# Optimization experiments

Measured on AMD Instinct MI355X. Metric: run time of the kernel, lower is better.

The kernel has to match this reference:

```python
import jax, jax.numpy as jnp
import numpy as np

N_PTS = 65536   # input points
M = 4096        # sampled clusters (n_nodes)
K = 16          # knn neighbors
C_IN = 128
C_OUT = 256
BN_EPS = 1e-5


def setup_inputs() -> dict:
    key = jax.random.key(0)
    k1, k2, k3 = jax.random.split(key, 3)
    x = jax.random.normal(k1, (N_PTS, C_IN), jnp.float32)
    pos = jax.random.normal(k2, (N_PTS, 3), jnp.float32)
    batch = jnp.zeros((N_PTS,), jnp.int32)  # single point cloud
    W = jax.random.normal(k3, (C_IN, C_OUT), jnp.float32) / np.sqrt(C_IN)
    b = jnp.zeros((C_OUT,), jnp.float32)
    gamma = jnp.ones((C_OUT,), jnp.float32)
    beta = jnp.zeros((C_OUT,), jnp.float32)
    return {"x": x, "pos": pos, "batch": batch, "W": W, "b": b,
            "gamma": gamma, "beta": beta}


def _fps(pos, m):
    """Farthest point sampling starting from index 0. Returns m indices."""
    n = pos.shape[0]

    def step(carry, _):
        min_d, last = carry
        d = jnp.sum((pos - pos[last]) ** 2, axis=-1)  # [N]
        min_d = jnp.minimum(min_d, d)
        nxt = jnp.argmax(min_d).astype(jnp.int32)
        return (min_d, nxt), nxt

    init = (jnp.full((n,), jnp.inf, pos.dtype), jnp.int32(0))
    _, rest = jax.lax.scan(step, init, None, length=m - 1)
    return jnp.concatenate([jnp.zeros((1,), jnp.int32), rest])


def _knn(pos, sub_pos, k):
    """For each of M query points, indices of k nearest points in pos. [M, k]"""
    # squared euclidean distances, [M, N]
    d2 = (jnp.sum(sub_pos ** 2, -1, keepdims=True)
          - 2.0 * sub_pos @ pos.T
          + jnp.sum(pos ** 2, -1)[None, :])
    _, idx = jax.lax.top_k(-d2, k)
    return idx


def _mlp(x, W, b, gamma, beta):
    # Linear -> BatchNorm1d (training-mode batch stats, biased var) -> ReLU
    h = x @ W + b                      # [N, C_OUT]
    mu = jnp.mean(h, axis=0)
    var = jnp.mean((h - mu) ** 2, axis=0)
    h = gamma * (h - mu) * jax.lax.rsqrt(var + BN_EPS) + beta
    return jax.nn.relu(h)


def reference(x, pos, batch, W, b, gamma, beta):
    id_clusters = _fps(pos, M)                 # [M]
    sub_pos = pos[id_clusters]                 # [M, 3]
    sub_batch = batch[id_clusters]             # [M]
    nbr = _knn(pos, sub_pos, K)                # [M, K]
    h = _mlp(x, W, b, gamma, beta)             # [N, C_OUT]
    # gather + max-pool over each cluster's k neighbors (== scatter_max,
    # since knn emits exactly K neighbors per cluster, grouped by cluster)
    out = jnp.max(h[nbr], axis=1)              # [M, C_OUT]
    return out, sub_pos, sub_batch
```

## Files before the change

### kernel.cpp

```cpp
#include <hip/hip_runtime.h>
#include <hip/hip_bf16.h>

#define N_PTS 65536
#define MCLUS 4096
#define KNN   16
#define C_IN  128
#define C_OUT 256

typedef unsigned long long u64;
typedef unsigned u32;

#define WS_ID     0
#define WS_SLOTS  16384
#define WS_NBR    49152
#define WS_PSUM   311296
#define WS_PSUMSQ 835584
#define WS_SCALE  1359872
#define WS_SHIFT  1360896

__global__ void init_kernel(int* __restrict__ id, u64* __restrict__ slots) {
    int t = threadIdx.x;
    for (int i = t; i < 4096; i += 1024) slots[i] = 0ull;
    if (t == 0) id[0] = 0;
}

__device__ __forceinline__ float dist3(float ax, float ay, float az,
                                       float bx, float by, float bz) {
    float dx = __fsub_rn(ax, bx), dy = __fsub_rn(ay, by), dz = __fsub_rn(az, bz);
    return __fadd_rn(__fadd_rn(__fmul_rn(dx, dx), __fmul_rn(dy, dy)), __fmul_rn(dz, dz));
}

__device__ __forceinline__ u32 wave_max_u32(u32 v) {
    #pragma unroll
    for (int off = 32; off > 0; off >>= 1) {
        u32 o = __shfl_xor(v, off);
        v = o > v ? o : v;
    }
    return v;
}

__device__ __forceinline__ int wave_argmax48(u64 k48) {
    u32 hi = (u32)(k48 >> 16);
    u32 him = wave_max_u32(hi);
    u64 ball = __ballot(hi == him);
    if (__popcll(ball) > 1) {
        u32 a = (hi == him) ? (u32)(k48 & 0xFFFFull) : 0u;
        u32 am = wave_max_u32(a);
        ball = __ballot((hi == him) && (a == am));
    }
    return __ffsll((long long)ball) - 1;
}

__global__ __launch_bounds__(64) void fps_kernel(const float* __restrict__ pos,
                                                 int* __restrict__ id,
                                                 u64* __restrict__ slots) {
    const int lane = threadIdx.x;
    const int blk  = blockIdx.x;
    __shared__ float bku[1024];

    float px[16], py[16], pz[16], md[16];
    const float c0x = pos[0], c0y = pos[1], c0z = pos[2];
    #pragma unroll
    for (int e = 0; e < 16; ++e) {
        int gi = blk * 1024 + e * 64 + lane;
        px[e] = pos[gi * 3 + 0]; py[e] = pos[gi * 3 + 1]; pz[e] = pos[gi * 3 + 2];
        md[e] = dist3(px[e], py[e], pz[e], c0x, c0y, c0z);
    }

    int r = 0;
    bool pending = false;

    auto slow_round = [&](int rr, int s) {
        u64 bk = 0; float bx = 0.f, by = 0.f, bz = 0.f;
        #pragma unroll
        for (int e = 0; e < 16; ++e) {
            u32 inv = 0xFFFFu - (u32)(blk * 1024 + e * 64 + lane);
            u64 k = ((u64)__float_as_uint(md[e]) << 16) | inv;
            bool bt = k > bk;
            bk = bt ? k : bk; bx = bt ? px[e] : bx; by = bt ? py[e] : by; bz = bt ? pz[e] : bz;
        }
        int src = wave_argmax48(bk);
        float wx = __shfl(bx, src), wy = __shfl(by, src), wz = __shfl(bz, src);
        u64 kb = __shfl(bk, src);

        const u64 tg = (u64)((rr + 1) & 0xFFFF);
        u64* base = &slots[(u32)(rr & 1) * 2048];
        {
            u64 w0 = (kb << 16) | tg;
            u64 w1 = ((u64)__float_as_uint(wx) << 32) | tg;
            u64 w2 = ((u64)__float_as_uint(wy) << 32) | tg;
            u64 w3 = ((u64)__float_as_uint(wz) << 32) | tg;
            u64 wv = (lane == 0) ? w0 : (lane == 1) ? w1 : (lane == 2) ? w2 : w3;
            if (lane < 4)
                __hip_atomic_store(&base[(u32)blk * 32 + (u32)lane], wv,
                                   __ATOMIC_RELAXED, __HIP_MEMORY_SCOPE_AGENT);
        }
        u64* bp = &base[(u32)lane * 32];
        u64 v0, v1, v2, v3;
        for (;;) {
            v0 = __hip_atomic_load(&bp[0], __ATOMIC_RELAXED, __HIP_MEMORY_SCOPE_AGENT);
            v1 = __hip_atomic_load(&bp[1], __ATOMIC_RELAXED, __HIP_MEMORY_SCOPE_AGENT);
            v2 = __hip_atomic_load(&bp[2], __ATOMIC_RELAXED, __HIP_MEMORY_SCOPE_AGENT);
            v3 = __hip_atomic_load(&bp[3], __ATOMIC_RELAXED, __HIP_MEMORY_SCOPE_AGENT);
            u64 bad = ((v0 ^ tg) | (v1 ^ tg) | (v2 ^ tg) | (v3 ^ tg)) & 0xFFFFull;
            if (bad == 0ull) break;
        }
        u64 k2 = v0 >> 16;
        int s2 = wave_argmax48(k2);
        u64 kw = __shfl(k2, s2);
        float cx = __shfl(__uint_as_float((u32)(v1 >> 32)), s2);
        float cy = __shfl(__uint_as_float((u32)(v2 >> 32)), s2);
        float cz = __shfl(__uint_as_float((u32)(v3 >> 32)), s2);
        if (blk == 0 && lane == 0) id[s] = (int)(0xFFFFu - (u32)(kw & 0xFFFFull));
        #pragma unroll
        for (int e = 0; e < 16; ++e)
            md[e] = fminf(md[e], dist3(px[e], py[e], pz[e], cx, cy, cz));
    };

    for (int B = 0; B <= 511; ++B) {
        u64 bk = 0; float bx = 0.f, by = 0.f, bz = 0.f;
        #pragma unroll
        for (int e = 0; e < 16; ++e) {
            u32 inv = 0xFFFFu - (u32)(blk * 1024 + e * 64 + lane);
            u64 k = ((u64)__float_as_uint(md[e]) << 16) | inv;
            bool bt = k > bk;
            bk = bt ? k : bk; bx = bt ? px[e] : bx; by = bt ? py[e] : by; bz = bt ? pz[e] : bz;
        }
        u64 ks = bk;
        #pragma unroll
        for (int off = 1; off <= 4; off <<= 1) {
            u64 o = __shfl_xor(ks, off);
            if (o > ks) ks = o;
        }
        {
            u64 ball = __ballot(bk == ks);
            int segbase = (lane >> 3) << 3;
            int ssrc = __ffsll((long long)(ball & (0xFFull << segbase))) - 1;
            bx = __shfl(bx, ssrc); by = __shfl(by, ssrc); bz = __shfl(bz, ssrc);
        }

        const u64 tg = (u64)((r + 1) & 0xFFFF);
        u64* base = &slots[(u32)(r & 1) * 2048];
        {
            int c = lane / 3; if (c > 7) c = 7;
            int p = lane - c * 3;
            int srcl = 8 * c;
            u64 kk  = __shfl(ks, srcl);
            float gx = __shfl(bx, srcl), gy = __shfl(by, srcl), gz = __shfl(bz, srcl);
            u32 hi, mid;
            if (p == 0)      { hi = __float_as_uint(gx); mid = (u32)(kk & 0xFFFFull); }
            else if (p == 1) { hi = __float_as_uint(gy); mid = (u32)(kk >> 32) & 0xFFFFu; }
            else             { hi = __float_as_uint(gz); mid = (u32)(kk >> 16) & 0xFFFFu; }
            u64 wd = ((u64)hi << 32) | ((u64)mid << 16) | tg;
            if (lane == 24) wd = ((u64)(pending ? 1u : 0u) << 16) | tg;
            if (lane < 25)
                __hip_atomic_store(&base[(u32)blk * 32 + (u32)lane], wd,
                                   __ATOMIC_RELAXED, __HIP_MEMORY_SCOPE_AGENT);
        }

        u64 w[25]; u32 valid = 0;
        {
            u64* bp = &base[(u32)lane * 32];
            do {
                #pragma unroll
                for (int i = 0; i < 25; ++i)
                    if (!(valid & (1u << i)))
                        w[i] = __hip_atomic_load(&bp[i], __ATOMIC_RELAXED, __HIP_MEMORY_SCOPE_AGENT);
                #pragma unroll
                for (int i = 0; i < 25; ++i)
                    if ((u32)(w[i] & 0xFFFFull) == (u32)tg) valid |= (1u << i);
            } while (valid != 0x1FFFFFFu);
        }
        ++r;

        bool anyviol = (__ballot(((w[24] >> 16) & 1ull) != 0ull) != 0ull);
        if (anyviol) {
            #pragma unroll
            for (int e = 0; e < 16; ++e) md[e] = bku[e * 64 + lane];
            int sbase = 8 * (B - 1) + 1;
            for (int sub = 0; sub < 8; ++sub) { slow_round(r, sbase + sub); ++r; }
            pending = false;
            --B; continue;
        }
        if (B == 511) break;

        float cpx[8], cpy[8], cpz[8], cmdf[8]; u32 cinv[8];
        #pragma unroll
        for (int c = 0; c < 8; ++c) {
            u64 a = w[3 * c], b = w[3 * c + 1], d = w[3 * c + 2];
            cpx[c] = __uint_as_float((u32)(a >> 32));
            cpy[c] = __uint_as_float((u32)(b >> 32));
            cpz[c] = __uint_as_float((u32)(d >> 32));
            cinv[c] = (u32)(a >> 16) & 0xFFFFu;
            u32 mdb = (((u32)(b >> 16) & 0xFFFFu) << 16) | ((u32)(d >> 16) & 0xFFFFu);
            cmdf[c] = __uint_as_float(mdb);
        }

        u64 wk48[8]; float wxa[8], wya[8], wza[8];
        float pwx = 0.f, pwy = 0.f, pwz = 0.f;
        #pragma unroll
        for (int j = 0; j < 8; ++j) {
            if (j) {
                #pragma unroll
                for (int c = 0; c < 8; ++c)
                    cmdf[c] = fminf(cmdf[c], dist3(cpx[c], cpy[c], cpz[c], pwx, pwy, pwz));
            }
            u64 bk2 = 0; float b2x = 0.f, b2y = 0.f, b2z = 0.f;
            #pragma unroll
            for (int c = 0; c < 8; ++c) {
                u64 k = ((u64)__float_as_uint(cmdf[c]) << 16) | cinv[c];
                bool bt = k > bk2;
                bk2 = bt ? k : bk2; b2x = bt ? cpx[c] : b2x; b2y = bt ? cpy[c] : b2y; b2z = bt ? cpz[c] : b2z;
            }
            int src = wave_argmax48(bk2);
            u64 kw = __shfl(bk2, src);
            float wx = __shfl(b2x, src), wy = __shfl(b2y, src), wz = __shfl(b2z, src);
            wk48[j] = kw; wxa[j] = wx; wya[j] = wy; wza[j] = wz;
            pwx = wx; pwy = wy; pwz = wz;
            if (blk == 0 && lane == 0) id[8 * B + 1 + j] = (int)(0xFFFFu - (u32)(kw & 0xFFFFull));
        }

        #pragma unroll
        for (int e = 0; e < 16; ++e) bku[e * 64 + lane] = md[e];
        bool viol = false;
        #pragma unroll
        for (int j = 0; j < 8; ++j) {
            #pragma unroll
            for (int e = 0; e < 16; ++e) {
                u32 inv = 0xFFFFu - (u32)(blk * 1024 + e * 64 + lane);
                u64 vk = ((u64)__float_as_uint(md[e]) << 16) | inv;
                viol |= (vk > wk48[j]);
            }
            #pragma unroll
            for (int e = 0; e < 16; ++e)
                md[e] = fminf(md[e], dist3(px[e], py[e], pz[e], wxa[j], wya[j], wza[j]));
        }
        pending = (__ballot(viol) != 0ull);
    }

    for (int s = 4089; s < 4096; ++s) { slow_round(r, s); ++r; }
}

__global__ void subout_kernel(const float* __restrict__ pos, const int* __restrict__ batch,
                              const int* __restrict__ id, float* __restrict__ sub_pos,
                              int* __restrict__ sub_batch) {
    int m = blockIdx.x * blockDim.x + threadIdx.x;
    if (m >= MCLUS) return;
    int idx = id[m];
    sub_pos[m*3+0] = pos[idx*3+0];
    sub_pos[m*3+1] = pos[idx*3+1];
    sub_pos[m*3+2] = pos[idx*3+2];
    sub_batch[m] = batch[idx];
}

__global__ __launch_bounds__(64) void knn_kernel(const float* __restrict__ pos,
                                                 const int* __restrict__ id,
                                                 int* __restrict__ nbr) {
    const int q = blockIdx.x;
    const int lane = threadIdx.x;
    const int qi = id[q];
    const float qx = pos[qi*3+0], qy = pos[qi*3+1], qz = pos[qi*3+2];
    const float nq = __fadd_rn(__fadd_rn(__fmul_rn(qx,qx), __fmul_rn(qy,qy)), __fmul_rn(qz,qz));

    float dl[KNN]; int il[KNN];
    #pragma unroll
    for (int t = 0; t < KNN; ++t) { dl[t] = __builtin_inff(); il[t] = 0x7FFFFFFF; }

    for (int j = lane; j < N_PTS; j += 64) {
        float px = pos[j*3+0], py = pos[j*3+1], pz = pos[j*3+2];
        float npj = __fadd_rn(__fadd_rn(__fmul_rn(px,px), __fmul_rn(py,py)), __fmul_rn(pz,pz));
        float dot = __fadd_rn(__fadd_rn(__fmul_rn(qx,px), __fmul_rn(qy,py)), __fmul_rn(qz,pz));
        float d2  = __fadd_rn(__fsub_rn(nq, __fmul_rn(2.0f, dot)), npj);
        if (d2 < dl[KNN-1] || (d2 == dl[KNN-1] && j < il[KNN-1])) {
            dl[KNN-1] = d2; il[KNN-1] = j;
            #pragma unroll
            for (int t = KNN-1; t > 0; --t) {
                float a = dl[t-1], bq = dl[t];
                int   ai = il[t-1], bi = il[t];
                bool sw = (bq < a) || (bq == a && bi < ai);
                dl[t-1] = sw ? bq : a;  dl[t] = sw ? a : bq;
                il[t-1] = sw ? bi : ai; il[t] = sw ? ai : bi;
            }
        }
    }

    __shared__ float sd[64][KNN];
    __shared__ int   si[64][KNN];
    #pragma unroll
    for (int t = 0; t < KNN; ++t) { sd[lane][t] = dl[t]; si[lane][t] = il[t]; }
    __syncthreads();

    int ptr = 0;
    for (int rr = 0; rr < KNN; ++rr) {
        unsigned long long key = ~0ull;
        if (ptr < KNN) {
            unsigned u = __float_as_uint(sd[lane][ptr]);
            unsigned mu = (u >> 31) ? ~u : (u | 0x80000000u);
            key = ((unsigned long long)mu << 32) | (unsigned)si[lane][ptr];
        }
        unsigned long long m = key;
        #pragma unroll
        for (int off = 32; off > 0; off >>= 1) {
            unsigned long long o = __shfl_xor(m, off);
            if (o < m) m = o;
        }
        if (key == m) ptr++;
        if (lane == 0) nbr[q*KNN + rr] = (int)(m & 0xFFFFFFFFull);
    }
}

__global__ __launch_bounds__(256) void stats_kernel(const float* __restrict__ x,
                                                    const float* __restrict__ W,
                                                    const float* __restrict__ b,
                                                    float* __restrict__ psum,
                                                    float* __restrict__ psumsq) {
    __shared__ float xl[64*128];
    const int tid = threadIdx.x;
    const int cg = (tid & 63) * 4;
    const int rq = tid >> 6;
    float s0=0,s1=0,s2v=0,s3=0, q0=0,q1=0,q2=0,q3=0;
    const float4 bv = *(const float4*)&b[cg];

    for (int t = 0; t < 2; ++t) {
        const size_t row0 = (size_t)blockIdx.x*128 + (size_t)t*64;
        __syncthreads();
        for (int i = tid*4; i < 64*128; i += 1024)
            *(float4*)&xl[i] = *(const float4*)&x[row0*128 + i];
        __syncthreads();

        float acc[16][4];
        #pragma unroll
        for (int rr = 0; rr < 16; ++rr) { acc[rr][0]=bv.x; acc[rr][1]=bv.y; acc[rr][2]=bv.z; acc[rr][3]=bv.w; }

        for (int k4 = 0; k4 < 32; ++k4) {
            float4 w0 = *(const float4*)&W[(k4*4+0)*256 + cg];
            float4 w1 = *(const float4*)&W[(k4*4+1)*256 + cg];
            float4 w2 = *(const float4*)&W[(k4*4+2)*256 + cg];
            float4 w3 = *(const float4*)&W[(k4*4+3)*256 + cg];
            #pragma unroll
            for (int rr = 0; rr < 16; ++rr) {
                float4 xv = *(float4*)&xl[(rq*16+rr)*128 + k4*4];
                acc[rr][0] = fmaf(xv.w,w3.x, fmaf(xv.z,w2.x, fmaf(xv.y,w1.x, fmaf(xv.x,w0.x, acc[rr][0]))));
                acc[rr][1] = fmaf(xv.w,w3.y, fmaf(xv.z,w2.y, fmaf(xv.y,w1.y, fmaf(xv.x,w0.y, acc[rr][1]))));
                acc[rr][2] = fmaf(xv.w,w3.z, fmaf(xv.z,w2.z, fmaf(xv.y,w1.z, fmaf(xv.x,w0.z, acc[rr][2]))));
                acc[rr][3] = fmaf(xv.w,w3.w, fmaf(xv.z,w2.w, fmaf(xv.y,w1.w, fmaf(xv.x,w0.w, acc[rr][3]))));
            }
        }
        #pragma unroll
        for (int rr = 0; rr < 16; ++rr) {
            s0 += acc[rr][0]; q0 = fmaf(acc[rr][0],acc[rr][0],q0);
            s1 += acc[rr][1]; q1 = fmaf(acc[rr][1],acc[rr][1],q1);
            s2v+= acc[rr][2]; q2 = fmaf(acc[rr][2],acc[rr][2],q2);
            s3 += acc[rr][3]; q3 = fmaf(acc[rr][3],acc[rr][3],q3);
        }
    }
    __syncthreads();
    float* red = xl;
    red[rq*256 + cg+0] = s0; red[rq*256 + cg+1] = s1; red[rq*256 + cg+2] = s2v; red[rq*256 + cg+3] = s3;
    red[1024 + rq*256 + cg+0] = q0; red[1024 + rq*256 + cg+1] = q1;
    red[1024 + rq*256 + cg+2] = q2; red[1024 + rq*256 + cg+3] = q3;
    __syncthreads();
    if (rq == 0) {
        #pragma unroll
        for (int c = 0; c < 4; ++c) {
            int ch = cg + c;
            float ss = red[ch] + red[256+ch] + red[512+ch] + red[768+ch];
            float qq = red[1024+ch] + red[1280+ch] + red[1536+ch] + red[1792+ch];
            psum  [blockIdx.x*256 + ch] = ss;
            psumsq[blockIdx.x*256 + ch] = qq;
        }
    }
}

__global__ void finalize_kernel(const float* __restrict__ psum, const float* __restrict__ psumsq,
                                const float* __restrict__ gamma, const float* __restrict__ beta,
                                float* __restrict__ scale, float* __restrict__ shift) {
    int c = threadIdx.x;
    float s = 0.f, s2 = 0.f;
    for (int bl = 0; bl < 512; ++bl) { s += psum[bl*256+c]; s2 += psumsq[bl*256+c]; }
    float mu  = s  / 65536.0f;
    float var = s2 / 65536.0f - mu*mu;
    float inv = rsqrtf(var + 1e-5f);
    float sc = gamma[c] * inv;
    scale[c] = sc;
    shift[c] = beta[c] - mu * sc;
}

__global__ __launch_bounds__(256) void out_kernel(const float* __restrict__ x,
                                                  const float* __restrict__ W,
                                                  const float* __restrict__ b,
                                                  const int* __restrict__ nbr,
                                                  const float* __restrict__ scale,
                                                  const float* __restrict__ shift,
                                                  float* __restrict__ out) {
    __shared__ float xl[16*128];
    __shared__ int nb[16];
    const int tid = threadIdx.x;
    const int m = blockIdx.x;
    if (tid < 16) nb[tid] = nbr[m*16 + tid];
    __syncthreads();
    for (int i = tid; i < 16*128; i += 256) {
        int rr = i >> 7, k = i & 127;
        xl[i] = x[(size_t)nb[rr]*128 + k];
    }
    __syncthreads();

    float acc[16];
    const float bias = b[tid];
    #pragma unroll
    for (int rr = 0; rr < 16; ++rr) acc[rr] = bias;

    for (int k4 = 0; k4 < 32; ++k4) {
        float w0 = W[(k4*4+0)*256 + tid];
        float w1 = W[(k4*4+1)*256 + tid];
        float w2 = W[(k4*4+2)*256 + tid];
        float w3 = W[(k4*4+3)*256 + tid];
        #pragma unroll
        for (int rr = 0; rr < 16; ++rr) {
            float4 xv = *(float4*)&xl[rr*128 + k4*4];
            acc[rr] = fmaf(xv.w,w3, fmaf(xv.z,w2, fmaf(xv.y,w1, fmaf(xv.x,w0, acc[rr]))));
        }
    }
    const float sc = scale[tid], sh = shift[tid];
    float v = acc[0];
    #pragma unroll
    for (int rr = 1; rr < 16; ++rr) v = (sc >= 0.f) ? fmaxf(v, acc[rr]) : fminf(v, acc[rr]);
    out[(size_t)m*256 + tid] = fmaxf(fmaf(sc, v, sh), 0.f);
}

extern "C" void kernel_launch(void* const* d_in, const int* in_sizes, int n_in,
                              void* d_out, int out_size, void* d_ws, size_t ws_size,
                              hipStream_t stream) {
    const float* x     = (const float*)d_in[0];
    const float* pos   = (const float*)d_in[1];
    const int*   batch = (const int*)  d_in[2];
    const float* W     = (const float*)d_in[3];
    const float* b     = (const float*)d_in[4];
    const float* gamma = (const float*)d_in[5];
    const float* beta  = (const float*)d_in[6];

    float* out      = (float*)d_out;
    float* sub_pos  = out + (size_t)MCLUS*C_OUT;
    int*   sub_batch= (int*)(out + (size_t)MCLUS*C_OUT + (size_t)MCLUS*3);

    char* ws = (char*)d_ws;
    int* id        = (int*)(ws + WS_ID);
    u64* slots     = (u64*)(ws + WS_SLOTS);
    int* nbr       = (int*)(ws + WS_NBR);
    float* psum    = (float*)(ws + WS_PSUM);
    float* psumsq  = (float*)(ws + WS_PSUMSQ);
    float* scalep  = (float*)(ws + WS_SCALE);
    float* shiftp  = (float*)(ws + WS_SHIFT);

    init_kernel<<<1, 1024, 0, stream>>>(id, slots);
    fps_kernel<<<64, 64, 0, stream>>>(pos, id, slots);
    subout_kernel<<<16, 256, 0, stream>>>(pos, batch, id, sub_pos, sub_batch);
    knn_kernel<<<MCLUS, 64, 0, stream>>>(pos, id, nbr);
    stats_kernel<<<512, 256, 0, stream>>>(x, W, b, psum, psumsq);
    finalize_kernel<<<1, 256, 0, stream>>>(psum, psumsq, gamma, beta, scalep, shiftp);
    out_kernel<<<MCLUS, 256, 0, stream>>>(x, W, b, nbr, scalep, shiftp, out);
}
```

Before: 7.569 ms.

## Spatially sort each FPS block's points into k-d cells before sampling

At kernel start, each FPS block sorts its 1024 points with three nested bitonic sorts in shared memory, by x, then y, then z, building a k-d style partition. Each 8-lane segment then holds a spatially compact group of points, and the original indices are precomputed for tie-breaking. The likely aim is to make the speculative per-segment candidate selection in the batched FPS loop more accurate, so fewer rounds hit violations and fall back to the slow path. The cost is an upfront sort with many __syncthreads barriers, extra shared memory, and 16 more registers per lane for the index array.

```diff
diff --git a/kernel.cpp b/kernel.cpp
--- a/kernel.cpp
+++ b/kernel.cpp
@@ -51,19 +51,70 @@
     return __ffsll((long long)ball) - 1;
 }
 
+__device__ __forceinline__ u32 fkey(float v) {
+    u32 u = __float_as_uint(v);
+    return (u >> 31) ? ~u : (u | 0x80000000u);
+}
+
+__device__ __forceinline__ void bsort_seg(u64* arr, int segsize, int lane) {
+    const int half = segsize >> 1;
+    for (int k = 2; k <= segsize; k <<= 1) {
+        for (int j = k >> 1; j > 0; j >>= 1) {
+            for (int t = lane; t < 512; t += 64) {
+                int seg = t / half;
+                int tt  = t - seg * half;
+                int io  = ((tt & ~(j - 1)) << 1) | (tt & (j - 1));
+                int i   = seg * segsize + io;
+                int l   = i | j;
+                u64 a = arr[i], b = arr[l];
+                bool up = ((io & k) == 0);
+                if ((a > b) == up) { arr[i] = b; arr[l] = a; }
+            }
+            __syncthreads();
+        }
+    }
+}
+
 __global__ __launch_bounds__(64) void fps_kernel(const float* __restrict__ pos,
                                                  int* __restrict__ id,
                                                  u64* __restrict__ slots) {
     const int lane = threadIdx.x;
     const int blk  = blockIdx.x;
+    __shared__ float sx[1024], sy[1024], sz[1024];
+    __shared__ u64  arr[1024];
     __shared__ float bku[1024];
 
+    for (int p = lane; p < 1024; p += 64) {
+        int gi = blk * 1024 + p;
+        sx[p] = pos[gi * 3 + 0]; sy[p] = pos[gi * 3 + 1]; sz[p] = pos[gi * 3 + 2];
+    }
+    __syncthreads();
+    for (int p = lane; p < 1024; p += 64)
+        arr[p] = ((u64)fkey(sx[p]) << 32) | (u32)p;
+    __syncthreads();
+    bsort_seg(arr, 1024, lane);
+    for (int p = lane; p < 1024; p += 64) {
+        u32 li = (u32)(arr[p] & 0xFFFFull);
+        arr[p] = ((u64)fkey(sy[li]) << 32) | li;
+    }
+    __syncthreads();
+    bsort_seg(arr, 512, lane);
+    for (int p = lane; p < 1024; p += 64) {
+        u32 li = (u32)(arr[p] & 0xFFFFull);
+        arr[p] = ((u64)fkey(sz[li]) << 32) | li;
+    }
+    __syncthreads();
+    bsort_seg(arr, 256, lane);
+
     float px[16], py[16], pz[16], md[16];
+    u32 inv[16];
     const float c0x = pos[0], c0y = pos[1], c0z = pos[2];
     #pragma unroll
     for (int e = 0; e < 16; ++e) {
-        int gi = blk * 1024 + e * 64 + lane;
-        px[e] = pos[gi * 3 + 0]; py[e] = pos[gi * 3 + 1]; pz[e] = pos[gi * 3 + 2];
+        int sp = (lane >> 3) * 128 + e * 8 + (lane & 7);
+        u32 li = (u32)(arr[sp] & 0xFFFFull);
+        px[e] = sx[li]; py[e] = sy[li]; pz[e] = sz[li];
+        inv[e] = 0xFFFFu - (u32)(blk * 1024 + (int)li);
         md[e] = dist3(px[e], py[e], pz[e], c0x, c0y, c0z);
     }
 
@@ -74,8 +125,7 @@
         u64 bk = 0; float bx = 0.f, by = 0.f, bz = 0.f;
         #pragma unroll
         for (int e = 0; e < 16; ++e) {
-            u32 inv = 0xFFFFu - (u32)(blk * 1024 + e * 64 + lane);
-            u64 k = ((u64)__float_as_uint(md[e]) << 16) | inv;
+            u64 k = ((u64)__float_as_uint(md[e]) << 16) | inv[e];
             bool bt = k > bk;
             bk = bt ? k : bk; bx = bt ? px[e] : bx; by = bt ? py[e] : by; bz = bt ? pz[e] : bz;
         }
@@ -121,8 +171,7 @@
         u64 bk = 0; float bx = 0.f, by = 0.f, bz = 0.f;
         #pragma unroll
         for (int e = 0; e < 16; ++e) {
-            u32 inv = 0xFFFFu - (u32)(blk * 1024 + e * 64 + lane);
-            u64 k = ((u64)__float_as_uint(md[e]) << 16) | inv;
+            u64 k = ((u64)__float_as_uint(md[e]) << 16) | inv[e];
             bool bt = k > bk;
             bk = bt ? k : bk; bx = bt ? px[e] : bx; by = bt ? py[e] : by; bz = bt ? pz[e] : bz;
         }
@@ -227,8 +276,7 @@
         for (int j = 0; j < 8; ++j) {
             #pragma unroll
             for (int e = 0; e < 16; ++e) {
-                u32 inv = 0xFFFFu - (u32)(blk * 1024 + e * 64 + lane);
-                u64 vk = ((u64)__float_as_uint(md[e]) << 16) | inv;
+                u64 vk = ((u64)__float_as_uint(md[e]) << 16) | inv[e];
                 viol |= (vk > wk48[j]);
             }
             #pragma unroll
```

Result: faster. 7.235 ms (-4.4%).

## Spatially sort points into Morton cells for FPS and resume fallback at first violation

Applied to the files above, without the earlier changes.

Adds bbox, count, scan and scatter kernels that bucket points into 512 Morton-ordered grid cells and store them as float4 with their original index. The FPS kernel then loads spatially coherent chunks per block, and the speculative 8-step batch records which step first failed, replaying only from that step instead of all eight. The aim is fewer speculation failures and cheaper recovery in the serial FPS loop. The cost is several extra small launches with atomics. The atomic-based scatter gives a nondeterministic point order within each cell, though tie-breaking still uses the original index.

```diff
diff --git a/kernel.cpp b/kernel.cpp
--- a/kernel.cpp
+++ b/kernel.cpp
@@ -12,16 +12,103 @@
 
 #define WS_ID     0
 #define WS_SLOTS  16384
-#define WS_NBR    49152
-#define WS_PSUM   311296
-#define WS_PSUMSQ 835584
-#define WS_SCALE  1359872
-#define WS_SHIFT  1360896
-
-__global__ void init_kernel(int* __restrict__ id, u64* __restrict__ slots) {
+#define WS_BBOX   49152
+#define WS_CNT    49216
+#define WS_OFS    51264
+#define WS_NBR    53312
+#define WS_PSUM   315456
+#define WS_POS4   315456
+#define WS_PSUMSQ 839744
+#define WS_SCALE  1364032
+#define WS_SHIFT  1365056
+
+__device__ __forceinline__ u32 fkey(float v) {
+    u32 u = __float_as_uint(v);
+    return (u >> 31) ? ~u : (u | 0x80000000u);
+}
+__device__ __forceinline__ float funkey(u32 k) {
+    u32 u = (k >> 31) ? (k & 0x7FFFFFFFu) : ~k;
+    return __uint_as_float(u);
+}
+
+__global__ void init_kernel(int* __restrict__ id, u64* __restrict__ slots,
+                            u32* __restrict__ bbox, int* __restrict__ cellcnt) {
     int t = threadIdx.x;
     for (int i = t; i < 4096; i += 1024) slots[i] = 0ull;
+    if (t < 512) cellcnt[t] = 0;
+    if (t < 3)   bbox[t] = 0xFFFFFFFFu;
+    if (t >= 3 && t < 6) bbox[t] = 0u;
     if (t == 0) id[0] = 0;
+}
+
+__global__ __launch_bounds__(256) void bbox_kernel(const float* __restrict__ pos,
+                                                   u32* __restrict__ bbox) {
+    int t = blockIdx.x * 256 + threadIdx.x;
+    u32 mn0 = 0xFFFFFFFFu, mn1 = 0xFFFFFFFFu, mn2 = 0xFFFFFFFFu;
+    u32 mx0 = 0u, mx1 = 0u, mx2 = 0u;
+    for (int i = t; i < N_PTS; i += 16384) {
+        u32 k0 = fkey(pos[i*3+0]), k1 = fkey(pos[i*3+1]), k2 = fkey(pos[i*3+2]);
+        mn0 = min(mn0, k0); mn1 = min(mn1, k1); mn2 = min(mn2, k2);
+        mx0 = max(mx0, k0); mx1 = max(mx1, k1); mx2 = max(mx2, k2);
+    }
+    #pragma unroll
+    for (int off = 32; off > 0; off >>= 1) {
+        mn0 = min(mn0, (u32)__shfl_xor(mn0, off)); mx0 = max(mx0, (u32)__shfl_xor(mx0, off));
+        mn1 = min(mn1, (u32)__shfl_xor(mn1, off)); mx1 = max(mx1, (u32)__shfl_xor(mx1, off));
+        mn2 = min(mn2, (u32)__shfl_xor(mn2, off)); mx2 = max(mx2, (u32)__shfl_xor(mx2, off));
+    }
+    if ((threadIdx.x & 63) == 0) {
+        atomicMin(&bbox[0], mn0); atomicMin(&bbox[1], mn1); atomicMin(&bbox[2], mn2);
+        atomicMax(&bbox[3], mx0); atomicMax(&bbox[4], mx1); atomicMax(&bbox[5], mx2);
+    }
+}
+
+__device__ __forceinline__ int cell_of(float x, float y, float z, const u32* bb) {
+    float x0 = funkey(bb[0]), y0 = funkey(bb[1]), z0 = funkey(bb[2]);
+    float x1 = funkey(bb[3]), y1 = funkey(bb[4]), z1 = funkey(bb[5]);
+    float sx = 8.0f / fmaxf(x1 - x0, 1e-20f);
+    float sy = 8.0f / fmaxf(y1 - y0, 1e-20f);
+    float sz = 8.0f / fmaxf(z1 - z0, 1e-20f);
+    int gx = min(max((int)((x - x0) * sx), 0), 7);
+    int gy = min(max((int)((y - y0) * sy), 0), 7);
+    int gz = min(max((int)((z - z0) * sz), 0), 7);
+    int m = 0;
+    #pragma unroll
+    for (int k = 0; k < 3; ++k)
+        m |= (((gx >> k) & 1) << (3*k + 2)) | (((gy >> k) & 1) << (3*k + 1)) | (((gz >> k) & 1) << (3*k));
+    return m;
+}
+
+__global__ __launch_bounds__(256) void count_kernel(const float* __restrict__ pos,
+                                                    const u32* __restrict__ bbox,
+                                                    int* __restrict__ cellcnt) {
+    int i = blockIdx.x * 256 + threadIdx.x;
+    atomicAdd(&cellcnt[cell_of(pos[i*3+0], pos[i*3+1], pos[i*3+2], bbox)], 1);
+}
+
+__global__ __launch_bounds__(512) void scan_kernel(const int* __restrict__ cellcnt,
+                                                   int* __restrict__ cellofs) {
+    __shared__ int tmp[512];
+    int t = threadIdx.x;
+    int c = cellcnt[t];
+    tmp[t] = c; __syncthreads();
+    for (int off = 1; off < 512; off <<= 1) {
+        int v = (t >= off) ? tmp[t - off] : 0;
+        __syncthreads();
+        tmp[t] += v;
+        __syncthreads();
+    }
+    cellofs[t] = tmp[t] - c;
+}
+
+__global__ __launch_bounds__(256) void scatter_kernel(const float* __restrict__ pos,
+                                                      const u32* __restrict__ bbox,
+                                                      int* __restrict__ cellofs,
+                                                      float4* __restrict__ pos4) {
+    int i = blockIdx.x * 256 + threadIdx.x;
+    float x = pos[i*3+0], y = pos[i*3+1], z = pos[i*3+2];
+    int o = atomicAdd(&cellofs[cell_of(x, y, z, bbox)], 1);
+    pos4[o] = make_float4(x, y, z, __int_as_float(i));
 }
 
 __device__ __forceinline__ float dist3(float ax, float ay, float az,
@@ -35,6 +122,14 @@
     for (int off = 32; off > 0; off >>= 1) {
         u32 o = __shfl_xor(v, off);
         v = o > v ? o : v;
+    }
+    return v;
+}
+__device__ __forceinline__ u32 wave_min_u32(u32 v) {
+    #pragma unroll
+    for (int off = 32; off > 0; off >>= 1) {
+        u32 o = __shfl_xor(v, off);
+        v = o < v ? o : v;
     }
     return v;
 }
@@ -52,6 +147,7 @@
 }
 
 __global__ __launch_bounds__(64) void fps_kernel(const float* __restrict__ pos,
+                                                 const float4* __restrict__ pos4,
                                                  int* __restrict__ id,
                                                  u64* __restrict__ slots) {
     const int lane = threadIdx.x;
@@ -59,23 +155,25 @@
     __shared__ float bku[1024];
 
     float px[16], py[16], pz[16], md[16];
+    u32 inv[16];
     const float c0x = pos[0], c0y = pos[1], c0z = pos[2];
     #pragma unroll
     for (int e = 0; e < 16; ++e) {
-        int gi = blk * 1024 + e * 64 + lane;
-        px[e] = pos[gi * 3 + 0]; py[e] = pos[gi * 3 + 1]; pz[e] = pos[gi * 3 + 2];
+        int sp = blk * 1024 + (lane >> 3) * 128 + e * 8 + (lane & 7);
+        float4 v = pos4[sp];
+        px[e] = v.x; py[e] = v.y; pz[e] = v.z;
+        inv[e] = 0xFFFFu - (u32)__float_as_int(v.w);
         md[e] = dist3(px[e], py[e], pz[e], c0x, c0y, c0z);
     }
 
     int r = 0;
-    bool pending = false;
+    u32 fb_mine = 0xFu;
 
     auto slow_round = [&](int rr, int s) {
         u64 bk = 0; float bx = 0.f, by = 0.f, bz = 0.f;
         #pragma unroll
         for (int e = 0; e < 16; ++e) {
-            u32 inv = 0xFFFFu - (u32)(blk * 1024 + e * 64 + lane);
-            u64 k = ((u64)__float_as_uint(md[e]) << 16) | inv;
+            u64 k = ((u64)__float_as_uint(md[e]) << 16) | inv[e];
             bool bt = k > bk;
             bk = bt ? k : bk; bx = bt ? px[e] : bx; by = bt ? py[e] : by; bz = bt ? pz[e] : bz;
         }
@@ -117,12 +215,13 @@
             md[e] = fminf(md[e], dist3(px[e], py[e], pz[e], cx, cy, cz));
     };
 
+    u64 wk48[8]; float wxa[8], wya[8], wza[8];
+
     for (int B = 0; B <= 511; ++B) {
         u64 bk = 0; float bx = 0.f, by = 0.f, bz = 0.f;
         #pragma unroll
         for (int e = 0; e < 16; ++e) {
-            u32 inv = 0xFFFFu - (u32)(blk * 1024 + e * 64 + lane);
-            u64 k = ((u64)__float_as_uint(md[e]) << 16) | inv;
+            u64 k = ((u64)__float_as_uint(md[e]) << 16) | inv[e];
             bool bt = k > bk;
             bk = bt ? k : bk; bx = bt ? px[e] : bx; by = bt ? py[e] : by; bz = bt ? pz[e] : bz;
         }
@@ -152,7 +251,7 @@
             else if (p == 1) { hi = __float_as_uint(gy); mid = (u32)(kk >> 32) & 0xFFFFu; }
             else             { hi = __float_as_uint(gz); mid = (u32)(kk >> 16) & 0xFFFFu; }
             u64 wd = ((u64)hi << 32) | ((u64)mid << 16) | tg;
-            if (lane == 24) wd = ((u64)(pending ? 1u : 0u) << 16) | tg;
+            if (lane == 24) wd = ((u64)(fb_mine & 0xFu) << 16) | tg;
             if (lane < 25)
                 __hip_atomic_store(&base[(u32)blk * 32 + (u32)lane], wd,
                                    __ATOMIC_RELAXED, __HIP_MEMORY_SCOPE_AGENT);
@@ -173,13 +272,21 @@
         }
         ++r;
 
-        bool anyviol = (__ballot(((w[24] >> 16) & 1ull) != 0ull) != 0ull);
-        if (anyviol) {
+        u32 jstar = wave_min_u32((u32)(w[24] >> 16) & 0xFu);
+        if (jstar < 8u) {
             #pragma unroll
             for (int e = 0; e < 16; ++e) md[e] = bku[e * 64 + lane];
+            #pragma unroll
+            for (int j = 0; j < 8; ++j) {
+                if ((u32)j < jstar) {
+                    #pragma unroll
+                    for (int e = 0; e < 16; ++e)
+                        md[e] = fminf(md[e], dist3(px[e], py[e], pz[e], wxa[j], wya[j], wza[j]));
+                }
+            }
             int sbase = 8 * (B - 1) + 1;
-            for (int sub = 0; sub < 8; ++sub) { slow_round(r, sbase + sub); ++r; }
-            pending = false;
+            for (int sub = (int)jstar; sub < 8; ++sub) { slow_round(r, sbase + sub); ++r; }
+            fb_mine = 0xFu;
             --B; continue;
         }
         if (B == 511) break;
@@ -196,7 +303,6 @@
             cmdf[c] = __uint_as_float(mdb);
         }
 
-        u64 wk48[8]; float wxa[8], wya[8], wza[8];
         float pwx = 0.f, pwy = 0.f, pwz = 0.f;
         #pragma unroll
         for (int j = 0; j < 8; ++j) {
@@ -222,20 +328,21 @@
 
         #pragma unroll
         for (int e = 0; e < 16; ++e) bku[e * 64 + lane] = md[e];
-        bool viol = false;
+        u32 vmask = 0;
         #pragma unroll
         for (int j = 0; j < 8; ++j) {
             #pragma unroll
             for (int e = 0; e < 16; ++e) {
-                u32 inv = 0xFFFFu - (u32)(blk * 1024 + e * 64 + lane);
-                u64 vk = ((u64)__float_as_uint(md[e]) << 16) | inv;
-                viol |= (vk > wk48[j]);
+                u64 vk = ((u64)__float_as_uint(md[e]) << 16) | inv[e];
+                if (vk > wk48[j]) vmask |= (1u << j);
             }
             #pragma unroll
             for (int e = 0; e < 16; ++e)
                 md[e] = fminf(md[e], dist3(px[e], py[e], pz[e], wxa[j], wya[j], wza[j]));
         }
-        pending = (__ballot(viol) != 0ull);
+        #pragma unroll
+        for (int off = 32; off > 0; off >>= 1) vmask |= (u32)__shfl_xor(vmask, off);
+        fb_mine = vmask ? (u32)(__ffs(vmask) - 1) : 0xFu;
     }
 
     for (int s = 4089; s < 4096; ++s) { slow_round(r, s); ++r; }
@@ -444,16 +551,24 @@
     int*   sub_batch= (int*)(out + (size_t)MCLUS*C_OUT + (size_t)MCLUS*3);
 
     char* ws = (char*)d_ws;
-    int* id        = (int*)(ws + WS_ID);
-    u64* slots     = (u64*)(ws + WS_SLOTS);
-    int* nbr       = (int*)(ws + WS_NBR);
-    float* psum    = (float*)(ws + WS_PSUM);
-    float* psumsq  = (float*)(ws + WS_PSUMSQ);
-    float* scalep  = (float*)(ws + WS_SCALE);
-    float* shiftp  = (float*)(ws + WS_SHIFT);
-
-    init_kernel<<<1, 1024, 0, stream>>>(id, slots);
-    fps_kernel<<<64, 64, 0, stream>>>(pos, id, slots);
+    int*    id      = (int*)   (ws + WS_ID);
+    u64*    slots   = (u64*)   (ws + WS_SLOTS);
+    u32*    bbox    = (u32*)   (ws + WS_BBOX);
+    int*    cellcnt = (int*)   (ws + WS_CNT);
+    int*    cellofs = (int*)   (ws + WS_OFS);
+    int*    nbr     = (int*)   (ws + WS_NBR);
+    float4* pos4    = (float4*)(ws + WS_POS4);
+    float*  psum    = (float*) (ws + WS_PSUM);
+    float*  psumsq  = (float*) (ws + WS_PSUMSQ);
+    float*  scalep  = (float*) (ws + WS_SCALE);
+    float*  shiftp  = (float*) (ws + WS_SHIFT);
+
+    init_kernel<<<1, 1024, 0, stream>>>(id, slots, bbox, cellcnt);
+    bbox_kernel<<<64, 256, 0, stream>>>(pos, bbox);
+    count_kernel<<<256, 256, 0, stream>>>(pos, bbox, cellcnt);
+    scan_kernel<<<1, 512, 0, stream>>>(cellcnt, cellofs);
+    scatter_kernel<<<256, 256, 0, stream>>>(pos, bbox, cellofs, pos4);
+    fps_kernel<<<64, 64, 0, stream>>>(pos, pos4, id, slots);
     subout_kernel<<<16, 256, 0, stream>>>(pos, batch, id, sub_pos, sub_batch);
     knn_kernel<<<MCLUS, 64, 0, stream>>>(pos, id, nbr);
     stats_kernel<<<512, 256, 0, stream>>>(x, W, b, psum, psumsq);
```

Result: slower. 7.865 ms (+3.9%).
